# Kernel tuning notes

Measured on AMD Instinct MI355X. Metric: run time of the kernel, lower is better.

Reference implementation:

```python
import jax, jax.numpy as jnp
import numpy as np

B, T, H, C = 1024, 1024, 128, 6  # batch, time, hidden_dim, output_dim


def setup_inputs() -> dict:
    key = jax.random.key(0)
    ks = jax.random.split(key, 16)
    xv = jax.random.normal(ks[0], (B, T, C), dtype=jnp.float32)
    m = (jax.random.uniform(ks[1], (B, T, C)) < 0.6).astype(jnp.float32)  # binary observed mask
    dt = jax.random.uniform(ks[2], (B, T, 1), dtype=jnp.float32) * 2.0    # positive time gaps
    x = jnp.concatenate([xv, m, dt], axis=-1)  # [B,T,13]
    s = 0.05
    return {
        "x": x,
        "x_mean": jnp.zeros((C,), jnp.float32),
        "decay_x_w": jnp.ones((C,), jnp.float32),
        "decay_x_b": jnp.zeros((C,), jnp.float32),
        "decay_h_w": jnp.ones((H,), jnp.float32),
        "decay_h_b": jnp.zeros((H,), jnp.float32),
        "w_ih": jax.random.normal(ks[3], (3 * H, 2 * C), jnp.float32) * s,
        "w_hh": jax.random.normal(ks[4], (3 * H, H), jnp.float32) * s,
        "b_ih": jnp.zeros((3 * H,), jnp.float32),
        "b_hh": jnp.zeros((3 * H,), jnp.float32),
        "w1": jax.random.normal(ks[5], (H, H), jnp.float32) * s,
        "b1": jnp.zeros((H,), jnp.float32),
        "w2": jax.random.normal(ks[6], (C, H), jnp.float32) * s,
        "b2": jnp.zeros((C,), jnp.float32),
        "wu1": jax.random.normal(ks[7], (H // 2, H), jnp.float32) * s,
        "bu1": jnp.zeros((H // 2,), jnp.float32),
        "wu2": jax.random.normal(ks[8], (C, H // 2), jnp.float32) * s,
        "bu2": jnp.zeros((C,), jnp.float32),
    }


def _grud_forward(x, x_mean, decay_x_w, decay_x_b, decay_h_w, decay_h_b,
                  w_ih, w_hh, b_ih, b_hh, w1, b1, w2, b2, wu1, bu1, wu2, bu2):
    xv = jnp.transpose(x[:, :, :C], (1, 0, 2))        # [T,B,C]
    m = jnp.transpose(x[:, :, C:2 * C], (1, 0, 2))    # [T,B,C]
    dt = jnp.transpose(x[:, :, 2 * C:2 * C + 1], (1, 0, 2))  # [T,B,1]

    def step(carry, inp):
        running, x_last, h = carry
        xv_t, m_t, dt_t = inp
        obs = m_t > 0.5
        running = jnp.where(obs, 0.0, running + dt_t)          # delta_t
        gamma_x = jnp.exp(-jax.nn.relu(running * decay_x_w + decay_x_b))  # [B,C]
        gamma_h = jnp.exp(-jax.nn.relu(dt_t * decay_h_w + decay_h_b))     # [B,H]
        h = gamma_h * h
        x_last = jnp.where(obs, xv_t, x_last)
        x_hat = m_t * xv_t + (1.0 - m_t) * (gamma_x * x_last + (1.0 - gamma_x) * x_mean)
        gru_in = jnp.concatenate([x_hat, m_t], axis=-1)        # [B,2C]
        gi = gru_in @ w_ih.T + b_ih                            # [B,3H]
        gh = h @ w_hh.T + b_hh                                 # [B,3H]
        i_r, i_z, i_n = jnp.split(gi, 3, axis=-1)
        h_r, h_z, h_n = jnp.split(gh, 3, axis=-1)
        r = jax.nn.sigmoid(i_r + h_r)
        z = jax.nn.sigmoid(i_z + h_z)
        n = jnp.tanh(i_n + r * h_n)
        h = (1.0 - z) * n + z * h
        pred = jax.nn.relu(h @ w1.T + b1) @ w2.T + b2
        unc = jax.nn.softplus(jax.nn.relu(h @ wu1.T + bu1) @ wu2.T + bu2)
        return (running, x_last, h), (pred, unc)

    bsz = x.shape[0]
    init = (jnp.zeros((bsz, C), x.dtype), jnp.zeros((bsz, C), x.dtype), jnp.zeros((bsz, H), x.dtype))
    _, (pred, unc) = jax.lax.scan(step, init, (xv, m, dt))
    return jnp.transpose(pred, (1, 0, 2)), jnp.transpose(unc, (1, 0, 2))


def reference(x, x_mean, decay_x_w, decay_x_b, decay_h_w, decay_h_b,
              w_ih, w_hh, b_ih, b_hh, w1, b1, w2, b2, wu1, bu1, wu2, bu2):
    return _grud_forward(x, x_mean, decay_x_w, decay_x_b, decay_h_w, decay_h_b,
                         w_ih, w_hh, b_ih, b_hh, w1, b1, w2, b2, wu1, bu1, wu2, bu2)
```

## Files before the change

kernel.cpp:

```cpp
#include <hip/hip_runtime.h>

namespace {
constexpr int NB = 1024, NT = 1024, NH = 128;
constexpr float L2E = 1.4426950408889634f;

typedef __bf16 bf16x8 __attribute__((ext_vector_type(8)));
typedef float  f32x4  __attribute__((ext_vector_type(4)));
typedef int    i32x4  __attribute__((ext_vector_type(4)));
union FRAG { i32x4 i; bf16x8 b; };

__device__ __forceinline__ unsigned short bfb(float f) {
  union { __bf16 h; unsigned short u; } c; c.h = (__bf16)f; return c.u;
}
__device__ __forceinline__ unsigned pkbf(float a, float b) {
  return (unsigned)bfb(a) | ((unsigned)bfb(b) << 16);
}
__device__ __forceinline__ unsigned long long pk4(const f32x4 v) {
  return (unsigned long long)pkbf(v[0], v[1]) |
         ((unsigned long long)pkbf(v[2], v[3]) << 32);
}
__device__ __forceinline__ float ex2(float x) { return __builtin_amdgcn_exp2f(x); }
__device__ __forceinline__ float rcp_(float x) { return __builtin_amdgcn_rcpf(x); }

__device__ __forceinline__ FRAG pk8(const float* pp, float sc) {
  FRAG f;
  #pragma unroll
  for (int j = 0; j < 4; ++j)
    f.i[j] = (int)pkbf(pp[2 * j] * sc, pp[2 * j + 1] * sc);
  return f;
}
}

#define MFMA(a, b, c) __builtin_amdgcn_mfma_f32_16x16x32_bf16(a, b, c, 0, 0, 0)
#define BAR() do { \
  asm volatile("s_waitcnt lgkmcnt(0)" ::: "memory"); \
  __builtin_amdgcn_s_barrier(); \
} while (0)

__global__ __launch_bounds__(512, 2)
void grud_combo(const float* __restrict__ x, const float* __restrict__ x_mean,
                const float* __restrict__ dxw, const float* __restrict__ dxb,
                const float* __restrict__ dhw, const float* __restrict__ dhb,
                const float* __restrict__ w_ih, const float* __restrict__ w_hh,
                const float* __restrict__ b_ih, const float* __restrict__ b_hh,
                const float* __restrict__ w1, const float* __restrict__ b1,
                const float* __restrict__ w2, const float* __restrict__ b2,
                const float* __restrict__ wu1, const float* __restrict__ bu1,
                const float* __restrict__ wu2, const float* __restrict__ bu2,
                float* __restrict__ out,
                char* __restrict__ hcur, const char* __restrict__ hprev,
                float* __restrict__ hstate, float* __restrict__ runst,
                float* __restrict__ xlst, int t0, int t0p, int Tc,
                int niter, int hb0)
{
  __shared__ __align__(16) char lds[40960];

  const int tid = threadIdx.x;
  const int lane = tid & 63, wv = tid >> 6;
  const int lr = lane & 15, lg = lane >> 4;

  if (t0 < NT && blockIdx.x < 64) {
    float (*xw)[16][17] = (float(*)[16][17])lds;
    char* ginB = lds + 2176;
    char* hdL  = lds + 4224;

    const int b0 = blockIdx.x * 16;
    const int uidx = wv * 16 + lr;
    const int uu0  = wv * 16 + 4 * lg;

    FRAG bhh[3][4], bgi[3];
    #pragma unroll
    for (int g = 0; g < 3; ++g) {
      const float sc = (g < 2) ? -L2E : 2.f * L2E;
      const int grow = g * 128 + uidx;
      const float* wrow = w_hh + (size_t)grow * NH;
      #pragma unroll
      for (int s = 0; s < 4; ++s) bhh[g][s] = pk8(wrow + 32 * s + 8 * lg, sc);
      FRAG f; f.i = i32x4{0, 0, 0, 0};
      if (lg < 2) {
        unsigned e[8];
        #pragma unroll
        for (int j = 0; j < 8; ++j) {
          const int c = 8 * lg + j; float v = 0.f;
          if (c < 12) {
            const int ch = c >> 1;
            v = ((c & 1) ? w_ih[(size_t)grow * 12 + 6 + ch]
                         : w_ih[(size_t)grow * 12 + ch]) * sc;
          } else if (c == 12) {
            v = ((g < 2) ? (b_ih[grow] + b_hh[grow]) : b_ih[grow]) * sc;
          }
          e[j] = bfb(v);
        }
        f.i[0] = (int)(e[0] | (e[1] << 16)); f.i[1] = (int)(e[2] | (e[3] << 16));
        f.i[2] = (int)(e[4] | (e[5] << 16)); f.i[3] = (int)(e[6] | (e[7] << 16));
      }
      bgi[g] = f;
    }
    f32x4 dhwV, dhbV, bhnV;
    #pragma unroll
    for (int r = 0; r < 4; ++r) {
      dhwV[r] = -L2E * dhw[uu0 + r];
      dhbV[r] = -L2E * dhb[uu0 + r];
      bhnV[r] = b_hh[256 + uu0 + r] * (2.f * L2E);
    }

    const int  item = wv * 24 + lane;
    const bool xl = (wv < 4) && (lane < 24);
    const int  xrow = item / 6, xch = item - 6 * (item / 6);
    float dxwS = 0.f, dxbS = 0.f, xm_l = 0.f, run = 0.f, xlast = 0.f;
    if (xl) {
      dxwS = -L2E * dxw[xch]; dxbS = -L2E * dxb[xch]; xm_l = x_mean[xch];
      if (t0 > 0) { run = runst[(b0 + xrow) * 6 + xch]; xlast = xlst[(b0 + xrow) * 6 + xch]; }
    }
    const int ginWo = (((2 * xch) >> 3) << 8) + xrow * 16 + ((2 * xch) & 7) * 2;

    const bool sl = (tid >= 256) && (tid < 464);
    const int sid = tid - 256;
    const int rrow = sid / 13, rcc = sid - 13 * (sid / 13);
    const float* xbase = x + (size_t)(b0 + rrow) * (NT * 13) + rcc;

    f32x4 hn = {0.f, 0.f, 0.f, 0.f};
    if (t0 > 0) hn = *(const f32x4*)&hstate[(size_t)(b0 + lr) * NH + uu0];

    const int wOff = (2 * wv + (lg >> 1)) * 256 + lr * 16 + (lg & 1) * 8;
    const int rBase = lane * 16;

    ((unsigned*)ginB)[tid] = 0u;

    const int cb0 = t0 & 1;
    if (sl) {
      xw[cb0][rrow][rcc]     = xbase[(size_t)t0 * 13];
      const int t1 = (t0 + 1 < NT) ? t0 + 1 : NT - 1;
      xw[cb0 ^ 1][rrow][rcc] = xbase[(size_t)t1 * 13];
    }
    __syncthreads();

    if (tid < 32) {
      const int par = tid >> 4, row = tid & 15;
      *(unsigned*)(ginB + par * 1024 + 256 + row * 16 + 8) = 0x00003F80u;
    }

    f32x4 hd;
    {
      const float dt0 = xw[cb0][lr][12];
      #pragma unroll
      for (int r = 0; r < 4; ++r)
        hd[r] = ex2(fminf(dt0 * dhwV[r] + dhbV[r], 0.f)) * hn[r];
      *(unsigned long long*)(hdL + cb0 * 4096 + wOff) = pk4(hd);
    }
    if (xl) {
      const float xv = xw[cb0][xrow][xch], mt = xw[cb0][xrow][6 + xch];
      const float dtv = xw[cb0][xrow][12];
      const bool obs = mt > 0.5f;
      run = obs ? 0.f : run + dtv;
      const float gx = ex2(fminf(run * dxwS + dxbS, 0.f));
      xlast = obs ? xv : xlast;
      const float xh = mt * xv + (1.f - mt) * (gx * xlast + (1.f - gx) * xm_l);
      *(unsigned*)(ginB + cb0 * 1024 + ginWo) = pkbf(xh, mt);
    }
    float xr2 = 0.f;
    if (sl) { const int t2 = (t0 + 2 < NT) ? t0 + 2 : NT - 1; xr2 = xbase[(size_t)t2 * 13]; }
    BAR();

    char* hwp = hcur + (((size_t)blockIdx.x * Tc) << 12) + wv * 32 + lg * 8 + lr * 256;
    const f32x4 z4 = {0.f, 0.f, 0.f, 0.f};
    const int tend = t0 + Tc;

    #pragma unroll 1
    for (int t = t0; t < tend; ++t) {
      const int p = t & 1, q = p ^ 1;

      const float dtn = xw[q][lr][12];
      f32x4 gmn;
      #pragma unroll
      for (int r = 0; r < 4; ++r)
        gmn[r] = ex2(fminf(dtn * dhwV[r] + dhbV[r], 0.f));

      FRAG ag; ag.i = *(const i32x4*)(ginB + p * 1024 + rBase);
      FRAG ah[4];
      #pragma unroll
      for (int s = 0; s < 4; ++s)
        ah[s].i = *(const i32x4*)(hdL + p * 4096 + s * 1024 + rBase);

      if (sl) {
        xw[p][rrow][rcc] = xr2;
        xr2 = xbase[(size_t)((t + 3 < NT) ? t + 3 : NT - 1) * 13];
      }

      f32x4 accr = MFMA(bgi[0].b, ag.b, z4);
      f32x4 accz = MFMA(bgi[1].b, ag.b, z4);
      f32x4 ani  = MFMA(bgi[2].b, ag.b, z4);
      f32x4 anh  = z4;
      #pragma unroll
      for (int s = 0; s < 4; ++s) {
        accr = MFMA(bhh[0][s].b, ah[s].b, accr);
        accz = MFMA(bhh[1][s].b, ah[s].b, accz);
        anh  = MFMA(bhh[2][s].b, ah[s].b, anh);
      }

      f32x4 hbv = anh + bhnV;
      float A[4];
      #pragma unroll
      for (int r = 0; r < 4; ++r) A[r] = 1.f + ex2(accr[r]);
      const float R01 = rcp_(A[0] * A[1]);
      const float R23 = rcp_(A[2] * A[3]);
      float rr[4];
      rr[0] = A[1] * R01; rr[1] = A[0] * R01;
      rr[2] = A[3] * R23; rr[3] = A[2] * R23;

      float num[4], den[4];
      #pragma unroll
      for (int r = 0; r < 4; ++r) {
        const float na = __builtin_fmaf(rr[r], hbv[r], ani[r]);
        const float En = ex2(na);
        const float Ez = ex2(accz[r]);
        const float ep1 = En + 1.f;
        num[r] = __builtin_fmaf(hd[r], ep1, (En - 1.f) * Ez);
        den[r] = ep1 * (1.f + Ez);
      }
      const float D01 = rcp_(den[0] * den[1]);
      const float D23 = rcp_(den[2] * den[3]);
      hn[0] = num[0] * den[1] * D01; hn[1] = num[1] * den[0] * D01;
      hn[2] = num[2] * den[3] * D23; hn[3] = num[3] * den[2] * D23;

      *(unsigned long long*)hwp = pk4(hn);
      hwp += 4096;

      #pragma unroll
      for (int r = 0; r < 4; ++r) hd[r] = gmn[r] * hn[r];
      *(unsigned long long*)(hdL + q * 4096 + wOff) = pk4(hd);

      if (xl && t + 1 < tend) {
        const float xv = xw[q][xrow][xch], mt = xw[q][xrow][6 + xch];
        const float dtv = xw[q][xrow][12];
        const bool obs = mt > 0.5f;
        run = obs ? 0.f : run + dtv;
        const float gx = ex2(fminf(run * dxwS + dxbS, 0.f));
        xlast = obs ? xv : xlast;
        const float xh = mt * xv + (1.f - mt) * (gx * xlast + (1.f - gx) * xm_l);
        *(unsigned*)(ginB + q * 1024 + ginWo) = pkbf(xh, mt);
      }
      BAR();
    }

    *(f32x4*)&hstate[(size_t)(b0 + lr) * NH + uu0] = hn;
    if (xl) { runst[(b0 + xrow) * 6 + xch] = run; xlst[(b0 + xrow) * 6 + xch] = xlast; }

  } else {
    if (t0p < 0) return;

    const int hb = blockIdx.x - hb0;
    const int nhb = (int)gridDim.x - hb0;
    const int tid2 = tid & 255, half = tid >> 8;
    const int lane2 = tid2 & 63, w4 = tid2 >> 6;
    const int lr2 = lane2 & 15, lg2 = lane2 >> 4;
    char* ldsH = lds + half * 20480;

    FRAG bw1a[4], bw1b[4], bq1[4], bw2[4], bq2[2];
    #pragma unroll
    for (int s = 0; s < 4; ++s) {
      bw1a[s] = pk8(w1 + (size_t)((2 * w4) * 16 + lr2) * 128 + 32 * s + 8 * lg2, 1.f);
      bw1b[s] = pk8(w1 + (size_t)((2 * w4 + 1) * 16 + lr2) * 128 + 32 * s + 8 * lg2, 1.f);
      bq1[s]  = pk8(wu1 + (size_t)(w4 * 16 + lr2) * 128 + 32 * s + 8 * lg2, 1.f);
      if (lr2 < 6) bw2[s] = pk8(w2 + (size_t)lr2 * 128 + 32 * s + 8 * lg2, 1.f);
      else         bw2[s].i = i32x4{0, 0, 0, 0};
      if (s < 2) {
        if (lr2 < 6) bq2[s] = pk8(wu2 + (size_t)lr2 * 64 + 32 * s + 8 * lg2, 1.f);
        else         bq2[s].i = i32x4{0, 0, 0, 0};
      }
    }
    const float b1a = b1[(2 * w4) * 16 + lr2], b1b = b1[(2 * w4 + 1) * 16 + lr2];
    const float bu1l = bu1[w4 * 16 + lr2];
    const float b2l = (lr2 < 6) ? b2[lr2] : 0.f, bu2l = (lr2 < 6) ? bu2[lr2] : 0.f;
    const f32x4 z4 = {0.f, 0.f, 0.f, 0.f};

    const int tc2 = Tc >> 1, total = 64 * tc2;
    const int cy0 = (2 * w4) * 16 + lr2, cy1 = (2 * w4 + 1) * 16 + lr2;
    const int cu = w4 * 16 + lr2;

    #pragma unroll 1
    for (int it = 0; it < niter; ++it) {
      const int hu = it * (nhb * 2) + hb * 2 + half;
      const bool valid = hu < total;
      int chain = 0, tp = 0;
      if (valid) { chain = hu / tc2; tp = hu - chain * tc2; }

      if (valid) {
        const char* src = hprev + (((size_t)chain * Tc + tp * 2) << 12);
        const int o = tid2 * 16, row = o >> 8, cell = (o >> 4) & 15;
        #pragma unroll
        for (int k2 = 0; k2 < 2; ++k2) {
          uint4 v = *(const uint4*)(src + k2 * 4096 + o);
          *(uint4*)(ldsH + k2 * 4096 + row * 256 + ((cell ^ (row & 7)) << 4)) = v;
        }
      }
      __syncthreads();

      if (valid) {
        #pragma unroll
        for (int k = 0; k < 2; ++k) {
          FRAG A[4];
          #pragma unroll
          for (int s = 0; s < 4; ++s)
            A[s].i = *(const i32x4*)(ldsH + k * 4096 + lr2 * 256 +
                                     (((4 * s + lg2) ^ (lr2 & 7)) << 4));
          f32x4 aa = z4, ab = z4, au = z4;
          #pragma unroll
          for (int s = 0; s < 4; ++s) {
            aa = MFMA(A[s].b, bw1a[s].b, aa);
            ab = MFMA(A[s].b, bw1b[s].b, ab);
            au = MFMA(A[s].b, bq1[s].b, au);
          }
          #pragma unroll
          for (int r = 0; r < 4; ++r) {
            const int m = k * 16 + 4 * lg2 + r;
            *(unsigned short*)(ldsH + 8192 + m * 256 + (((cy0 >> 3) ^ (m & 7)) << 4) +
                               (cy0 & 7) * 2) = bfb(fmaxf(aa[r] + b1a, 0.f));
            *(unsigned short*)(ldsH + 8192 + m * 256 + (((cy1 >> 3) ^ (m & 7)) << 4) +
                               (cy1 & 7) * 2) = bfb(fmaxf(ab[r] + b1b, 0.f));
            *(unsigned short*)(ldsH + 16384 + m * 128 + (((cu >> 3) ^ (m & 7)) << 4) +
                               (cu & 7) * 2) = bfb(fmaxf(au[r] + bu1l, 0.f));
          }
        }
      }
      __syncthreads();

      if (valid && w4 < 2) {
        const int mrow = w4 * 16 + lr2;
        FRAG Y[4], U[2];
        #pragma unroll
        for (int s = 0; s < 4; ++s)
          Y[s].i = *(const i32x4*)(ldsH + 8192 + mrow * 256 +
                                   (((4 * s + lg2) ^ (lr2 & 7)) << 4));
        #pragma unroll
        for (int s = 0; s < 2; ++s)
          U[s].i = *(const i32x4*)(ldsH + 16384 + mrow * 128 +
                                   (((4 * s + lg2) ^ (lr2 & 7)) << 4));
        f32x4 ap = z4, aq = z4;
        #pragma unroll
        for (int s = 0; s < 4; ++s) ap = MFMA(Y[s].b, bw2[s].b, ap);
        #pragma unroll
        for (int s = 0; s < 2; ++s) aq = MFMA(U[s].b, bq2[s].b, aq);

        if (lr2 < 6) {
          const int t = t0p + tp * 2 + w4;
          #pragma unroll
          for (int r = 0; r < 4; ++r) {
            const int b = chain * 16 + 4 * lg2 + r;
            const size_t o = ((size_t)b * NT + t) * 6 + lr2;
            out[o] = ap[r] + b2l;
            const float xa = aq[r] + bu2l;
            const float sp = fmaxf(xa, 0.f) + 0.6931471805599453f *
                __builtin_amdgcn_logf(1.f + ex2(-fabsf(xa) * L2E));
            out[(size_t)NB * NT * 6 + o] = sp;
          }
        }
      }
      __syncthreads();
    }
  }
}

extern "C" void kernel_launch(void* const* d_in, const int* in_sizes, int n_in,
                              void* d_out, int out_size, void* d_ws, size_t ws_size,
                              hipStream_t stream) {
  (void)in_sizes; (void)n_in; (void)out_size;
  const float* p[18];
  for (int i = 0; i < 18; ++i) p[i] = (const float*)d_in[i];

  const size_t STATE = (size_t)1024 * 128 * 4 + 2 * (size_t)1024 * 6 * 4;
  int Tc = 256;
  while (Tc > 16 && (2 * ((size_t)Tc << 18) + STATE) > ws_size) Tc >>= 1;

  char* h0 = (char*)d_ws;
  char* h1 = h0 + ((size_t)Tc << 18);
  float* hstate = (float*)(h1 + ((size_t)Tc << 18));
  float* runst = hstate + 1024 * 128;
  float* xlst = runst + 1024 * 6;

  const int nch = NT / Tc;
  const int total = 64 * (Tc / 2);

  for (int k = 0; k <= nch; ++k) {
    char* hcur = (k & 1) ? h1 : h0;
    const char* hprev = (k & 1) ? h0 : h1;
    const int t0 = k * Tc;
    const int hb0 = (t0 < NT) ? 64 : 0;
    const int stride = (512 - hb0) * 2;
    const int niter = (total + stride - 1) / stride;
    hipLaunchKernelGGL(grud_combo, dim3(512), dim3(512), 0, stream,
                       p[0], p[1], p[2], p[3], p[4], p[5], p[6], p[7], p[8], p[9],
                       p[10], p[11], p[12], p[13], p[14], p[15], p[16], p[17],
                       (float*)d_out, hcur, hprev, hstate, runst, xlst,
                       t0, (k - 1) * Tc, Tc, niter, hb0);
  }
}
```

Measured before the change: 826.9 us.

## Add dedicated helper waves for input prep and widen head blocks to three halves

Raises the block size from 512 to 768 threads. In the recurrence blocks, the first 8 waves do only the GRU MFMA math, while 4 extra waves handle x-hat preparation and the global prefetch of upcoming x rows, taking that work off the critical serial path. In the output-head blocks, each block now processes three h-tiles per iteration instead of two, using the enlarged 60KB LDS. The cost is more registers and LDS per block, which may lower occupancy, and the helper waves add barrier participants to every step.

```diff
diff --git a/kernel.cpp b/kernel.cpp
--- a/kernel.cpp
+++ b/kernel.cpp
@@ -37,7 +37,7 @@
   __builtin_amdgcn_s_barrier(); \
 } while (0)
 
-__global__ __launch_bounds__(512, 2)
+__global__ __launch_bounds__(768, 2)
 void grud_combo(const float* __restrict__ x, const float* __restrict__ x_mean,
                 const float* __restrict__ dxw, const float* __restrict__ dxb,
                 const float* __restrict__ dhw, const float* __restrict__ dhb,
@@ -53,7 +53,7 @@
                 float* __restrict__ xlst, int t0, int t0p, int Tc,
                 int niter, int hb0)
 {
-  __shared__ __align__(16) char lds[40960];
+  __shared__ __align__(16) char lds[61440];
 
   const int tid = threadIdx.x;
   const int lane = tid & 63, wv = tid >> 6;
@@ -65,48 +65,51 @@
     char* hdL  = lds + 4224;
 
     const int b0 = blockIdx.x * 16;
-    const int uidx = wv * 16 + lr;
-    const int uu0  = wv * 16 + 4 * lg;
+    const bool gw = tid < 512;
+    const int uidx = (wv & 7) * 16 + lr;
+    const int uu0  = (wv & 7) * 16 + 4 * lg;
 
     FRAG bhh[3][4], bgi[3];
-    #pragma unroll
-    for (int g = 0; g < 3; ++g) {
-      const float sc = (g < 2) ? -L2E : 2.f * L2E;
-      const int grow = g * 128 + uidx;
-      const float* wrow = w_hh + (size_t)grow * NH;
+    f32x4 dhwV = {0.f,0.f,0.f,0.f}, dhbV = {0.f,0.f,0.f,0.f}, bhnV = {0.f,0.f,0.f,0.f};
+    if (gw) {
       #pragma unroll
-      for (int s = 0; s < 4; ++s) bhh[g][s] = pk8(wrow + 32 * s + 8 * lg, sc);
-      FRAG f; f.i = i32x4{0, 0, 0, 0};
-      if (lg < 2) {
-        unsigned e[8];
-        #pragma unroll
-        for (int j = 0; j < 8; ++j) {
-          const int c = 8 * lg + j; float v = 0.f;
-          if (c < 12) {
-            const int ch = c >> 1;
-            v = ((c & 1) ? w_ih[(size_t)grow * 12 + 6 + ch]
-                         : w_ih[(size_t)grow * 12 + ch]) * sc;
-          } else if (c == 12) {
-            v = ((g < 2) ? (b_ih[grow] + b_hh[grow]) : b_ih[grow]) * sc;
+      for (int g = 0; g < 3; ++g) {
+        const float sc = (g < 2) ? -L2E : 2.f * L2E;
+        const int grow = g * 128 + uidx;
+        const float* wrow = w_hh + (size_t)grow * NH;
+        #pragma unroll
+        for (int s = 0; s < 4; ++s) bhh[g][s] = pk8(wrow + 32 * s + 8 * lg, sc);
+        FRAG f; f.i = i32x4{0, 0, 0, 0};
+        if (lg < 2) {
+          unsigned e[8];
+          #pragma unroll
+          for (int j = 0; j < 8; ++j) {
+            const int c = 8 * lg + j; float v = 0.f;
+            if (c < 12) {
+              const int ch = c >> 1;
+              v = ((c & 1) ? w_ih[(size_t)grow * 12 + 6 + ch]
+                           : w_ih[(size_t)grow * 12 + ch]) * sc;
+            } else if (c == 12) {
+              v = ((g < 2) ? (b_ih[grow] + b_hh[grow]) : b_ih[grow]) * sc;
+            }
+            e[j] = bfb(v);
           }
-          e[j] = bfb(v);
-        }
-        f.i[0] = (int)(e[0] | (e[1] << 16)); f.i[1] = (int)(e[2] | (e[3] << 16));
-        f.i[2] = (int)(e[4] | (e[5] << 16)); f.i[3] = (int)(e[6] | (e[7] << 16));
-      }
-      bgi[g] = f;
-    }
-    f32x4 dhwV, dhbV, bhnV;
-    #pragma unroll
-    for (int r = 0; r < 4; ++r) {
-      dhwV[r] = -L2E * dhw[uu0 + r];
-      dhbV[r] = -L2E * dhb[uu0 + r];
-      bhnV[r] = b_hh[256 + uu0 + r] * (2.f * L2E);
-    }
-
-    const int  item = wv * 24 + lane;
-    const bool xl = (wv < 4) && (lane < 24);
-    const int  xrow = item / 6, xch = item - 6 * (item / 6);
+          f.i[0] = (int)(e[0] | (e[1] << 16)); f.i[1] = (int)(e[2] | (e[3] << 16));
+          f.i[2] = (int)(e[4] | (e[5] << 16)); f.i[3] = (int)(e[6] | (e[7] << 16));
+        }
+        bgi[g] = f;
+      }
+      #pragma unroll
+      for (int r = 0; r < 4; ++r) {
+        dhwV[r] = -L2E * dhw[uu0 + r];
+        dhbV[r] = -L2E * dhb[uu0 + r];
+        bhnV[r] = b_hh[256 + uu0 + r] * (2.f * L2E);
+      }
+    }
+
+    const int hid = tid - 512;
+    const bool xl = (hid >= 0) && (hid < 96);
+    const int xrow = (hid >= 0) ? hid / 6 : 0, xch = (hid >= 0) ? hid - 6 * (hid / 6) : 0;
     float dxwS = 0.f, dxbS = 0.f, xm_l = 0.f, run = 0.f, xlast = 0.f;
     if (xl) {
       dxwS = -L2E * dxw[xch]; dxbS = -L2E * dxb[xch]; xm_l = x_mean[xch];
@@ -114,24 +117,28 @@
     }
     const int ginWo = (((2 * xch) >> 3) << 8) + xrow * 16 + ((2 * xch) & 7) * 2;
 
-    const bool sl = (tid >= 256) && (tid < 464);
-    const int sid = tid - 256;
-    const int rrow = sid / 13, rcc = sid - 13 * (sid / 13);
-    const float* xbase = x + (size_t)(b0 + rrow) * (NT * 13) + rcc;
+    const bool st_ = (hid >= 96) && (hid < 200);
+    const int sid = (hid >= 96) ? hid - 96 : 0;
+    const int r1r = sid / 13, r1c = sid - 13 * r1r;
+    const int r2r = (sid + 104) / 13, r2c = (sid + 104) - 13 * ((sid + 104) / 13);
+    const float* xb1 = x + (size_t)(b0 + r1r) * (NT * 13) + r1c;
+    const float* xb2 = x + (size_t)(b0 + r2r) * (NT * 13) + r2c;
 
     f32x4 hn = {0.f, 0.f, 0.f, 0.f};
-    if (t0 > 0) hn = *(const f32x4*)&hstate[(size_t)(b0 + lr) * NH + uu0];
-
-    const int wOff = (2 * wv + (lg >> 1)) * 256 + lr * 16 + (lg & 1) * 8;
+    if (gw && t0 > 0) hn = *(const f32x4*)&hstate[(size_t)(b0 + lr) * NH + uu0];
+
+    const int wOff = (2 * (wv & 7) + (lg >> 1)) * 256 + lr * 16 + (lg & 1) * 8;
     const int rBase = lane * 16;
 
-    ((unsigned*)ginB)[tid] = 0u;
+    if (tid < 512) ((unsigned*)ginB)[tid] = 0u;
 
     const int cb0 = t0 & 1;
-    if (sl) {
-      xw[cb0][rrow][rcc]     = xbase[(size_t)t0 * 13];
+    if (st_) {
       const int t1 = (t0 + 1 < NT) ? t0 + 1 : NT - 1;
-      xw[cb0 ^ 1][rrow][rcc] = xbase[(size_t)t1 * 13];
+      xw[cb0][r1r][r1c]     = xb1[(size_t)t0 * 13];
+      xw[cb0 ^ 1][r1r][r1c] = xb1[(size_t)t1 * 13];
+      xw[cb0][r2r][r2c]     = xb2[(size_t)t0 * 13];
+      xw[cb0 ^ 1][r2r][r2c] = xb2[(size_t)t1 * 13];
     }
     __syncthreads();
 
@@ -140,8 +147,8 @@
       *(unsigned*)(ginB + par * 1024 + 256 + row * 16 + 8) = 0x00003F80u;
     }
 
-    f32x4 hd;
-    {
+    f32x4 hd = {0.f, 0.f, 0.f, 0.f};
+    if (gw) {
       const float dt0 = xw[cb0][lr][12];
       #pragma unroll
       for (int r = 0; r < 4; ++r)
@@ -158,11 +165,14 @@
       const float xh = mt * xv + (1.f - mt) * (gx * xlast + (1.f - gx) * xm_l);
       *(unsigned*)(ginB + cb0 * 1024 + ginWo) = pkbf(xh, mt);
     }
-    float xr2 = 0.f;
-    if (sl) { const int t2 = (t0 + 2 < NT) ? t0 + 2 : NT - 1; xr2 = xbase[(size_t)t2 * 13]; }
+    float xr2a = 0.f, xr2b = 0.f;
+    if (st_) {
+      const int t2 = (t0 + 2 < NT) ? t0 + 2 : NT - 1;
+      xr2a = xb1[(size_t)t2 * 13]; xr2b = xb2[(size_t)t2 * 13];
+    }
     BAR();
 
-    char* hwp = hcur + (((size_t)blockIdx.x * Tc) << 12) + wv * 32 + lg * 8 + lr * 256;
+    char* hwp = hcur + (((size_t)blockIdx.x * Tc) << 12) + (wv & 7) * 32 + lg * 8 + lr * 256;
     const f32x4 z4 = {0.f, 0.f, 0.f, 0.f};
     const int tend = t0 + Tc;
 
@@ -170,80 +180,82 @@
     for (int t = t0; t < tend; ++t) {
       const int p = t & 1, q = p ^ 1;
 
-      const float dtn = xw[q][lr][12];
-      f32x4 gmn;
-      #pragma unroll
-      for (int r = 0; r < 4; ++r)
-        gmn[r] = ex2(fminf(dtn * dhwV[r] + dhbV[r], 0.f));
-
-      FRAG ag; ag.i = *(const i32x4*)(ginB + p * 1024 + rBase);
-      FRAG ah[4];
-      #pragma unroll
-      for (int s = 0; s < 4; ++s)
-        ah[s].i = *(const i32x4*)(hdL + p * 4096 + s * 1024 + rBase);
-
-      if (sl) {
-        xw[p][rrow][rcc] = xr2;
-        xr2 = xbase[(size_t)((t + 3 < NT) ? t + 3 : NT - 1) * 13];
-      }
-
-      f32x4 accr = MFMA(bgi[0].b, ag.b, z4);
-      f32x4 accz = MFMA(bgi[1].b, ag.b, z4);
-      f32x4 ani  = MFMA(bgi[2].b, ag.b, z4);
-      f32x4 anh  = z4;
-      #pragma unroll
-      for (int s = 0; s < 4; ++s) {
-        accr = MFMA(bhh[0][s].b, ah[s].b, accr);
-        accz = MFMA(bhh[1][s].b, ah[s].b, accz);
-        anh  = MFMA(bhh[2][s].b, ah[s].b, anh);
-      }
-
-      f32x4 hbv = anh + bhnV;
-      float A[4];
-      #pragma unroll
-      for (int r = 0; r < 4; ++r) A[r] = 1.f + ex2(accr[r]);
-      const float R01 = rcp_(A[0] * A[1]);
-      const float R23 = rcp_(A[2] * A[3]);
-      float rr[4];
-      rr[0] = A[1] * R01; rr[1] = A[0] * R01;
-      rr[2] = A[3] * R23; rr[3] = A[2] * R23;
-
-      float num[4], den[4];
-      #pragma unroll
-      for (int r = 0; r < 4; ++r) {
-        const float na = __builtin_fmaf(rr[r], hbv[r], ani[r]);
-        const float En = ex2(na);
-        const float Ez = ex2(accz[r]);
-        const float ep1 = En + 1.f;
-        num[r] = __builtin_fmaf(hd[r], ep1, (En - 1.f) * Ez);
-        den[r] = ep1 * (1.f + Ez);
-      }
-      const float D01 = rcp_(den[0] * den[1]);
-      const float D23 = rcp_(den[2] * den[3]);
-      hn[0] = num[0] * den[1] * D01; hn[1] = num[1] * den[0] * D01;
-      hn[2] = num[2] * den[3] * D23; hn[3] = num[3] * den[2] * D23;
-
-      *(unsigned long long*)hwp = pk4(hn);
+      if (gw) {
+        const float dtn = xw[q][lr][12];
+        f32x4 gmn;
+        #pragma unroll
+        for (int r = 0; r < 4; ++r)
+          gmn[r] = ex2(fminf(dtn * dhwV[r] + dhbV[r], 0.f));
+
+        FRAG ag; ag.i = *(const i32x4*)(ginB + p * 1024 + rBase);
+        FRAG ah[4];
+        #pragma unroll
+        for (int s = 0; s < 4; ++s)
+          ah[s].i = *(const i32x4*)(hdL + p * 4096 + s * 1024 + rBase);
+
+        f32x4 accr = MFMA(bgi[0].b, ag.b, z4);
+        f32x4 accz = MFMA(bgi[1].b, ag.b, z4);
+        f32x4 ani  = MFMA(bgi[2].b, ag.b, z4);
+        f32x4 anh  = z4;
+        #pragma unroll
+        for (int s = 0; s < 4; ++s) {
+          accr = MFMA(bhh[0][s].b, ah[s].b, accr);
+          accz = MFMA(bhh[1][s].b, ah[s].b, accz);
+          anh  = MFMA(bhh[2][s].b, ah[s].b, anh);
+        }
+
+        f32x4 hbv = anh + bhnV;
+        float A[4];
+        #pragma unroll
+        for (int r = 0; r < 4; ++r) A[r] = 1.f + ex2(accr[r]);
+        const float R01 = rcp_(A[0] * A[1]);
+        const float R23 = rcp_(A[2] * A[3]);
+        float rr[4];
+        rr[0] = A[1] * R01; rr[1] = A[0] * R01;
+        rr[2] = A[3] * R23; rr[3] = A[2] * R23;
+
+        float num[4], den[4];
+        #pragma unroll
+        for (int r = 0; r < 4; ++r) {
+          const float na = __builtin_fmaf(rr[r], hbv[r], ani[r]);
+          const float En = ex2(na);
+          const float Ez = ex2(accz[r]);
+          const float ep1 = En + 1.f;
+          num[r] = __builtin_fmaf(hd[r], ep1, (En - 1.f) * Ez);
+          den[r] = ep1 * (1.f + Ez);
+        }
+        const float D01 = rcp_(den[0] * den[1]);
+        const float D23 = rcp_(den[2] * den[3]);
+        hn[0] = num[0] * den[1] * D01; hn[1] = num[1] * den[0] * D01;
+        hn[2] = num[2] * den[3] * D23; hn[3] = num[3] * den[2] * D23;
+
+        *(unsigned long long*)hwp = pk4(hn);
+
+        #pragma unroll
+        for (int r = 0; r < 4; ++r) hd[r] = gmn[r] * hn[r];
+        *(unsigned long long*)(hdL + q * 4096 + wOff) = pk4(hd);
+      } else {
+        if (xl && t + 1 < tend) {
+          const float xv = xw[q][xrow][xch], mt = xw[q][xrow][6 + xch];
+          const float dtv = xw[q][xrow][12];
+          const bool obs = mt > 0.5f;
+          run = obs ? 0.f : run + dtv;
+          const float gx = ex2(fminf(run * dxwS + dxbS, 0.f));
+          xlast = obs ? xv : xlast;
+          const float xh = mt * xv + (1.f - mt) * (gx * xlast + (1.f - gx) * xm_l);
+          *(unsigned*)(ginB + q * 1024 + ginWo) = pkbf(xh, mt);
+        }
+        if (st_) {
+          const int t3 = (t + 3 < NT) ? t + 3 : NT - 1;
+          xw[p][r1r][r1c] = xr2a; xr2a = xb1[(size_t)t3 * 13];
+          xw[p][r2r][r2c] = xr2b; xr2b = xb2[(size_t)t3 * 13];
+        }
+      }
       hwp += 4096;
-
-      #pragma unroll
-      for (int r = 0; r < 4; ++r) hd[r] = gmn[r] * hn[r];
-      *(unsigned long long*)(hdL + q * 4096 + wOff) = pk4(hd);
-
-      if (xl && t + 1 < tend) {
-        const float xv = xw[q][xrow][xch], mt = xw[q][xrow][6 + xch];
-        const float dtv = xw[q][xrow][12];
-        const bool obs = mt > 0.5f;
-        run = obs ? 0.f : run + dtv;
-        const float gx = ex2(fminf(run * dxwS + dxbS, 0.f));
-        xlast = obs ? xv : xlast;
-        const float xh = mt * xv + (1.f - mt) * (gx * xlast + (1.f - gx) * xm_l);
-        *(unsigned*)(ginB + q * 1024 + ginWo) = pkbf(xh, mt);
-      }
       BAR();
     }
 
-    *(f32x4*)&hstate[(size_t)(b0 + lr) * NH + uu0] = hn;
+    if (gw) *(f32x4*)&hstate[(size_t)(b0 + lr) * NH + uu0] = hn;
     if (xl) { runst[(b0 + xrow) * 6 + xch] = run; xlst[(b0 + xrow) * 6 + xch] = xlast; }
 
   } else {
@@ -280,7 +292,7 @@
 
     #pragma unroll 1
     for (int it = 0; it < niter; ++it) {
-      const int hu = it * (nhb * 2) + hb * 2 + half;
+      const int hu = it * (nhb * 3) + hb * 3 + half;
       const bool valid = hu < total;
       int chain = 0, tp = 0;
       if (valid) { chain = hu / tc2; tp = hu - chain * tc2; }
@@ -386,9 +398,9 @@
     const char* hprev = (k & 1) ? h0 : h1;
     const int t0 = k * Tc;
     const int hb0 = (t0 < NT) ? 64 : 0;
-    const int stride = (512 - hb0) * 2;
+    const int stride = (512 - hb0) * 3;
     const int niter = (total + stride - 1) / stride;
-    hipLaunchKernelGGL(grud_combo, dim3(512), dim3(512), 0, stream,
+    hipLaunchKernelGGL(grud_combo, dim3(512), dim3(768), 0, stream,
                        p[0], p[1], p[2], p[3], p[4], p[5], p[6], p[7], p[8], p[9],
                        p[10], p[11], p[12], p[13], p[14], p[15], p[16], p[17],
                        (float*)d_out, hcur, hprev, hstate, runst, xlst,
```

New measurement: 860.8 us. +4.1%, slower.
